# Kernel optimization log

Hardware: AMD Instinct MI355X
Metric: run time of the kernel (lower is better)

The kernel has to match this reference:

```python
import jax, jax.numpy as jnp
import numpy as np

TOP_K = 8  # num_experts_per_tok


def setup_inputs() -> dict:
    key = jax.random.key(0)
    k1, k2, k3 = jax.random.split(key, 3)
    B, S, H, E = 4, 4096, 2048, 64
    hidden_states = jax.random.normal(k1, (B, S, H), dtype=jnp.float32)
    router_weight = jax.random.normal(k2, (E, H), dtype=jnp.float32)
    router_bias = jnp.zeros((E,), dtype=jnp.float32)
    expert_bias = jax.random.normal(k3, (E, H), dtype=jnp.float32) * 0.1
    return {
        "hidden_states": hidden_states,
        "router_weight": router_weight,
        "router_bias": router_bias,
        "expert_bias": expert_bias,
    }


def reference(hidden_states, router_weight, router_bias, expert_bias):
    B, S, H = hidden_states.shape
    flat = hidden_states.reshape(B * S, H)  # [T, H]
    # Router: linear -> softmax -> top-k
    logits = jnp.einsum("th,eh->te", flat, router_weight) + router_bias
    scores = jax.nn.softmax(logits, axis=-1)
    topk_w, topk_idx = jax.lax.top_k(scores, TOP_K)  # [T, K]
    # Dispatch/combine collapses to: combined[t,k] = x[t] + expert_bias[idx[t,k]]
    # output[t] = sum_k w[t,k] * combined[t,k]
    #          = x[t] * sum_k w[t,k] + sum_k w[t,k] * expert_bias[idx[t,k]]
    gathered_bias = expert_bias[topk_idx]  # [T, K, H]
    out = flat * jnp.sum(topk_w, axis=-1, keepdims=True) + jnp.einsum(
        "tk,tkh->th", topk_w, gathered_bias
    )
    return out.reshape(B, S, H)
```

## Files before the change

### kernel.cpp

```cpp
#include <hip/hip_runtime.h>
#include <hip/hip_bf16.h>
#include <float.h>

#define H 2048
#define E 64
#define TOPK 8
#define TT 16
#define NT 512

typedef __attribute__((ext_vector_type(8))) short bf16x8;
typedef __attribute__((ext_vector_type(4))) float f32x4;
typedef __attribute__((ext_vector_type(4))) unsigned short us4;

__device__ __forceinline__ unsigned short f2bf(float f) {
  unsigned u = __float_as_uint(f);
  u += 0x7fffu + ((u >> 16) & 1u);
  return (unsigned short)(u >> 16);
}
__device__ __forceinline__ float bf2f(unsigned short s) {
  return __uint_as_float(((unsigned)s) << 16);
}
__device__ __forceinline__ float wred_max(float v) {
#pragma unroll
  for (int o = 32; o > 0; o >>= 1) v = fmaxf(v, __shfl_xor(v, o));
  return v;
}
__device__ __forceinline__ float wred_sum(float v) {
#pragma unroll
  for (int o = 32; o > 0; o >>= 1) v += __shfl_xor(v, o);
  return v;
}

__global__ __launch_bounds__(256) void cvt_kernel(const float* __restrict__ W,
                                                  const float* __restrict__ eb,
                                                  unsigned short* __restrict__ Wb,
                                                  unsigned short* __restrict__ Bb) {
  int i = (blockIdx.x * 256 + threadIdx.x) * 4;
  const float* src;
  unsigned short* dst;
  int off;
  if (i < E * H) { src = W; dst = Wb; off = i; }
  else           { src = eb; dst = Bb; off = i - E * H; }
  float4 v = *(const float4*)(src + off);
  us4 r;
  r[0] = f2bf(v.x); r[1] = f2bf(v.y); r[2] = f2bf(v.z); r[3] = f2bf(v.w);
  *(us4*)(dst + off) = r;
}

template <bool USE_WS>
__global__ __launch_bounds__(NT, 4) void moe_kernel(
    const float* __restrict__ x, const float* __restrict__ W,
    const float* __restrict__ rb, const float* __restrict__ eb,
    const unsigned short* __restrict__ Wb, const unsigned short* __restrict__ Bb,
    float* __restrict__ out) {
  __shared__ unsigned short xl[TT][H + 8];
  __shared__ float lg[TT][E + 1];
  __shared__ float msw[TT];
  __shared__ float mw[TT][TOPK];
  __shared__ int   mi[TT][TOPK];

  const int tid = threadIdx.x;
  const int t0  = blockIdx.x * TT;
  const int wv = tid >> 6, lane = tid & 63, quad = lane >> 4, m = lane & 15;

  {
    const int r0 = wv * 2;
#pragma unroll
    for (int rr = 0; rr < 2; ++rr) {
      const float* row = x + (size_t)(t0 + r0 + rr) * H;
#pragma unroll
      for (int i = 0; i < 8; ++i) {
        const int c = (i * 64 + lane) * 4;
        float4 a = *(const float4*)(row + c);
        us4 ra;
        ra[0] = f2bf(a.x); ra[1] = f2bf(a.y); ra[2] = f2bf(a.z); ra[3] = f2bf(a.w);
        *(us4*)&xl[r0 + rr][c] = ra;
      }
    }
  }
  __syncthreads();

  if (wv < 4) {
    const int e = wv * 16 + m;
    f32x4 acc = {0.f, 0.f, 0.f, 0.f};
    const unsigned short* xp = &xl[m][quad * 8];
    if (USE_WS) {
      const unsigned short* wp = Wb + (size_t)e * H + quad * 8;
#pragma unroll 8
      for (int it = 0; it < H / 32; ++it) {
        bf16x8 av = *(const bf16x8*)(xp + it * 32);
        bf16x8 bv = *(const bf16x8*)(wp + it * 32);
        acc = __builtin_amdgcn_mfma_f32_16x16x32_bf16(av, bv, acc, 0, 0, 0);
      }
    } else {
      const float* wp = W + (size_t)e * H + quad * 8;
#pragma unroll 4
      for (int it = 0; it < H / 32; ++it) {
        bf16x8 av = *(const bf16x8*)(xp + it * 32);
        float4 p = *(const float4*)(wp + it * 32);
        float4 q = *(const float4*)(wp + it * 32 + 4);
        bf16x8 bv;
        bv[0] = (short)f2bf(p.x); bv[1] = (short)f2bf(p.y);
        bv[2] = (short)f2bf(p.z); bv[3] = (short)f2bf(p.w);
        bv[4] = (short)f2bf(q.x); bv[5] = (short)f2bf(q.y);
        bv[6] = (short)f2bf(q.z); bv[7] = (short)f2bf(q.w);
        acc = __builtin_amdgcn_mfma_f32_16x16x32_bf16(av, bv, acc, 0, 0, 0);
      }
    }
#pragma unroll
    for (int r = 0; r < 4; ++r) lg[quad * 4 + r][wv * 16 + m] = acc[r];
  }
  __syncthreads();

  {
#pragma unroll
    for (int tt = 0; tt < 2; ++tt) {
      const int t = wv * 2 + tt;
      float l = lg[t][lane] + rb[lane];
      const float mx = wred_max(l);
      const float p = expf(l - mx);
      const float inv = 1.f / wred_sum(p);
      float sumw = 0.f;
      float lsel = l;
#pragma unroll
      for (int k = 0; k < TOPK; ++k) {
        const float mk = wred_max(lsel);
        const unsigned long long b = __ballot(lsel == mk);
        const int idx = __ffsll(b) - 1;
        const float wk = expf(mk - mx) * inv;
        sumw += wk;
        if (lane == 0) { mw[t][k] = wk; mi[t][k] = idx; }
        if (lane == idx) lsel = -FLT_MAX;
      }
      if (lane == 0) msw[t] = sumw;
    }
  }
  __syncthreads();

  {
    const int c = tid * 4;
    for (int t = 0; t < TT; ++t) {
      const float sw = msw[t];
      us4 xv = *(const us4*)&xl[t][c];
      float o[4];
#pragma unroll
      for (int i = 0; i < 4; ++i) o[i] = bf2f(xv[i]) * sw;
#pragma unroll
      for (int k = 0; k < TOPK; ++k) {
        const int e = mi[t][k];
        const float wk = mw[t][k];
        if (USE_WS) {
          us4 bv = *(const us4*)(Bb + (size_t)e * H + c);
#pragma unroll
          for (int i = 0; i < 4; ++i) o[i] += wk * bf2f(bv[i]);
        } else {
          float4 p = *(const float4*)(eb + (size_t)e * H + c);
          o[0] += wk * p.x; o[1] += wk * p.y; o[2] += wk * p.z; o[3] += wk * p.w;
        }
      }
      *(float4*)(out + (size_t)(t0 + t) * H + c) = make_float4(o[0], o[1], o[2], o[3]);
    }
  }
}

extern "C" void kernel_launch(void* const* d_in, const int* in_sizes, int n_in,
                              void* d_out, int out_size, void* d_ws, size_t ws_size,
                              hipStream_t stream) {
  const float* x  = (const float*)d_in[0];
  const float* W  = (const float*)d_in[1];
  const float* rb = (const float*)d_in[2];
  const float* eb = (const float*)d_in[3];
  float* out = (float*)d_out;

  const int T = in_sizes[0] / H;
  const int grid = T / TT;

  const size_t need = (size_t)2 * E * H * sizeof(unsigned short);
  if (ws_size >= need) {
    unsigned short* Wb = (unsigned short*)d_ws;
    unsigned short* Bb = Wb + E * H;
    cvt_kernel<<<(2 * E * H) / (256 * 4), 256, 0, stream>>>(W, eb, Wb, Bb);
    moe_kernel<true><<<grid, NT, 0, stream>>>(x, W, rb, eb, Wb, Bb, out);
  } else {
    moe_kernel<false><<<grid, NT, 0, stream>>>(x, W, rb, eb, nullptr, nullptr, out);
  }
}
```

Baseline: 285.7 us.

## Halve token tile, split router GEMM over K across all waves, widen combine

Drops tokens per block from 16 to 8 and raises the occupancy hint to 8, so there are twice as many blocks and more can be resident per CU. All 8 waves now compute the router GEMM, each covering half of H; the partial logits are summed in shared memory. The combine stage handles 8 columns per thread with two token groups, and the expert offset is precomputed as idx*H. The cost is that half the MFMA rows are wasted, since only 8 of 16 are valid, and each block re-reads W for fewer tokens.

```diff
diff --git a/kernel.cpp b/kernel.cpp
--- a/kernel.cpp
+++ b/kernel.cpp
@@ -5,7 +5,7 @@
 #define H 2048
 #define E 64
 #define TOPK 8
-#define TT 16
+#define TT 8
 #define NT 512
 
 typedef __attribute__((ext_vector_type(8))) short bf16x8;
@@ -48,13 +48,13 @@
 }
 
 template <bool USE_WS>
-__global__ __launch_bounds__(NT, 4) void moe_kernel(
+__global__ __launch_bounds__(NT, 8) void moe_kernel(
     const float* __restrict__ x, const float* __restrict__ W,
     const float* __restrict__ rb, const float* __restrict__ eb,
     const unsigned short* __restrict__ Wb, const unsigned short* __restrict__ Bb,
     float* __restrict__ out) {
   __shared__ unsigned short xl[TT][H + 8];
-  __shared__ float lg[TT][E + 1];
+  __shared__ float lgp[2][TT][E + 1];
   __shared__ float msw[TT];
   __shared__ float mw[TT][TOPK];
   __shared__ int   mi[TT][TOPK];
@@ -64,38 +64,36 @@
   const int wv = tid >> 6, lane = tid & 63, quad = lane >> 4, m = lane & 15;
 
   {
-    const int r0 = wv * 2;
-#pragma unroll
-    for (int rr = 0; rr < 2; ++rr) {
-      const float* row = x + (size_t)(t0 + r0 + rr) * H;
-#pragma unroll
-      for (int i = 0; i < 8; ++i) {
-        const int c = (i * 64 + lane) * 4;
-        float4 a = *(const float4*)(row + c);
-        us4 ra;
-        ra[0] = f2bf(a.x); ra[1] = f2bf(a.y); ra[2] = f2bf(a.z); ra[3] = f2bf(a.w);
-        *(us4*)&xl[r0 + rr][c] = ra;
-      }
+    const float* row = x + (size_t)(t0 + wv) * H;
+#pragma unroll
+    for (int i = 0; i < 8; ++i) {
+      const int c = (i * 64 + lane) * 4;
+      float4 a = *(const float4*)(row + c);
+      us4 ra;
+      ra[0] = f2bf(a.x); ra[1] = f2bf(a.y); ra[2] = f2bf(a.z); ra[3] = f2bf(a.w);
+      *(us4*)&xl[wv][c] = ra;
     }
   }
   __syncthreads();
 
-  if (wv < 4) {
-    const int e = wv * 16 + m;
+  {
+    const int eg = wv & 3, kh = wv >> 2;
+    const int e = eg * 16 + m;
+    const int k0 = kh * (H / 2);
     f32x4 acc = {0.f, 0.f, 0.f, 0.f};
-    const unsigned short* xp = &xl[m][quad * 8];
+    const unsigned short* xp = &xl[m & 7][k0 + quad * 8];
     if (USE_WS) {
-      const unsigned short* wp = Wb + (size_t)e * H + quad * 8;
+      const unsigned short* wp = Wb + (size_t)e * H + k0 + quad * 8;
 #pragma unroll 8
-      for (int it = 0; it < H / 32; ++it) {
+      for (int it = 0; it < H / 64; ++it) {
         bf16x8 av = *(const bf16x8*)(xp + it * 32);
         bf16x8 bv = *(const bf16x8*)(wp + it * 32);
         acc = __builtin_amdgcn_mfma_f32_16x16x32_bf16(av, bv, acc, 0, 0, 0);
       }
     } else {
-      const float* wp = W + (size_t)e * H + quad * 8;
+      const float* wp = W + (size_t)e * H + k0 + quad * 8;
 #pragma unroll 4
-      for (int it = 0; it < H / 32; ++it) {
+      for (int it = 0; it < H / 64; ++it) {
         bf16x8 av = *(const bf16x8*)(xp + it * 32);
         float4 p = *(const float4*)(wp + it * 32);
         float4 q = *(const float4*)(wp + it * 32 + 4);
@@ -108,57 +106,72 @@
       }
     }
 #pragma unroll
-    for (int r = 0; r < 4; ++r) lg[quad * 4 + r][wv * 16 + m] = acc[r];
+    for (int r = 0; r < 4; ++r) {
+      const int row = quad * 4 + r;
+      if (row < TT) lgp[kh][row][eg * 16 + m] = acc[r];
+    }
   }
   __syncthreads();
 
   {
-#pragma unroll
-    for (int tt = 0; tt < 2; ++tt) {
-      const int t = wv * 2 + tt;
-      float l = lg[t][lane] + rb[lane];
-      const float mx = wred_max(l);
-      const float p = expf(l - mx);
-      const float inv = 1.f / wred_sum(p);
-      float sumw = 0.f;
-      float lsel = l;
+    const int t = wv;
+    float l = lgp[0][t][lane] + lgp[1][t][lane] + rb[lane];
+    const float mx = wred_max(l);
+    const float p = expf(l - mx);
+    const float inv = 1.f / wred_sum(p);
+    float sumw = 0.f;
+    float lsel = l;
+#pragma unroll
+    for (int k = 0; k < TOPK; ++k) {
+      const float mk = wred_max(lsel);
+      const unsigned long long b = __ballot(lsel == mk);
+      const int idx = __ffsll(b) - 1;
+      const float wk = expf(mk - mx) * inv;
+      sumw += wk;
+      if (lane == 0) { mw[t][k] = wk; mi[t][k] = idx * H; }
+      if (lane == idx) lsel = -FLT_MAX;
+    }
+    if (lane == 0) msw[t] = sumw;
+  }
+  __syncthreads();
+
+  {
+    const int tg = tid >> 8;
+    const int c8 = (tid & 255) * 8;
+    const unsigned short* bbase = Bb + c8;
+    const float* ebase = eb + c8;
+#pragma unroll 1
+    for (int tt = 0; tt < TT / 2; ++tt) {
+      const int t = tg * (TT / 2) + tt;
+      const float sw = msw[t];
+      const float4 w0 = *(const float4*)&mw[t][0];
+      const float4 w1 = *(const float4*)&mw[t][4];
+      const int4  e0 = *(const int4*)&mi[t][0];
+      const int4  e1 = *(const int4*)&mi[t][4];
+      const float wks[8] = {w0.x, w0.y, w0.z, w0.w, w1.x, w1.y, w1.z, w1.w};
+      const int   ofs[8] = {e0.x, e0.y, e0.z, e0.w, e1.x, e1.y, e1.z, e1.w};
+      bf16x8 xv = *(const bf16x8*)&xl[t][c8];
+      float o[8];
+#pragma unroll
+      for (int i = 0; i < 8; ++i) o[i] = bf2f((unsigned short)xv[i]) * sw;
 #pragma unroll
       for (int k = 0; k < TOPK; ++k) {
-        const float mk = wred_max(lsel);
-        const unsigned long long b = __ballot(lsel == mk);
-        const int idx = __ffsll(b) - 1;
-        const float wk = expf(mk - mx) * inv;
-        sumw += wk;
-        if (lane == 0) { mw[t][k] = wk; mi[t][k] = idx; }
-        if (lane == idx) lsel = -FLT_MAX;
-      }
-      if (lane == 0) msw[t] = sumw;
-    }
-  }
-  __syncthreads();
-
-  {
-    const int c = tid * 4;
-    for (int t = 0; t < TT; ++t) {
-      const float sw = msw[t];
-      us4 xv = *(const us4*)&xl[t][c];
-      float o[4];
-#pragma unroll
-      for (int i = 0; i < 4; ++i) o[i] = bf2f(xv[i]) * sw;
-#pragma unroll
-      for (int k = 0; k < TOPK; ++k) {
-        const int e = mi[t][k];
-        const float wk = mw[t][k];
+        const float wk = wks[k];
         if (USE_WS) {
-          us4 bv = *(const us4*)(Bb + (size_t)e * H + c);
-#pragma unroll
-          for (int i = 0; i < 4; ++i) o[i] += wk * bf2f(bv[i]);
+          bf16x8 bv = *(const bf16x8*)(bbase + ofs[k]);
+#pragma unroll
+          for (int i = 0; i < 8; ++i) o[i] += wk * bf2f((unsigned short)bv[i]);
         } else {
-          float4 p = *(const float4*)(eb + (size_t)e * H + c);
-          o[0] += wk * p.x; o[1] += wk * p.y; o[2] += wk * p.z; o[3] += wk * p.w;
+          const float* p = ebase + ofs[k];
+          float4 p0 = *(const float4*)p;
+          float4 p1 = *(const float4*)(p + 4);
+          o[0] += wk * p0.x; o[1] += wk * p0.y; o[2] += wk * p0.z; o[3] += wk * p0.w;
+          o[4] += wk * p1.x; o[5] += wk * p1.y; o[6] += wk * p1.z; o[7] += wk * p1.w;
         }
       }
-      *(float4*)(out + (size_t)(t0 + t) * H + c) = make_float4(o[0], o[1], o[2], o[3]);
+      float* op = out + (size_t)(t0 + t) * H + c8;
+      *(float4*)op       = make_float4(o[0], o[1], o[2], o[3]);
+      *(float4*)(op + 4) = make_float4(o[4], o[5], o[6], o[7]);
     }
   }
 }
```

Result: no change. 289.3 us (+1.3%).
